# Kernel optimization log

Hardware: AMD Instinct MI355X
Metric: run time of the kernel (lower is better)

## Reference

```python
import jax, jax.numpy as jnp
import numpy as np

TAU = 0.5

def setup_inputs() -> dict:
    key = jax.random.key(0)
    kx, ky = jax.random.split(key)
    B, H = 8192, 256
    x = jax.random.normal(kx, (B, H), dtype=jnp.float32)
    y = jax.random.normal(ky, (B, H), dtype=jnp.float32)
    return {"x": x, "y": y}

def reference(x, y):
    # L2-normalize rows
    x_norm = x / jnp.linalg.norm(x, axis=1, keepdims=True)
    y_norm = y / jnp.linalg.norm(y, axis=1, keepdims=True)
    xy_norm = jnp.concatenate([x_norm, y_norm], axis=0)  # [2N, H]
    yx_norm = jnp.concatenate([y_norm, x_norm], axis=0)  # [2N, H]
    # [2N, 2N] cosine-similarity matrix (dominant memory traffic)
    sim_mat_1 = xy_norm @ xy_norm.T
    exp_mat = jnp.exp(sim_mat_1 / TAU)
    exp_row_sum = jnp.sum(exp_mat, axis=1)
    exp_diag = jnp.diagonal(exp_mat)
    denominator = exp_row_sum - exp_diag
    # diag(xy_norm @ yx_norm.T) is the row-wise dot product (avoids redundant NxN matmul)
    pos_sim = jnp.sum(xy_norm * yx_norm, axis=1)
    numerator = jnp.exp(pos_sim / TAU)
    nt_xent = -jnp.log(numerator / denominator)
    return jnp.mean(nt_xent)
```

## Files before the change

kernel.cpp:

```cpp
#include <hip/hip_runtime.h>
#include <hip/hip_bf16.h>
#include <math.h>

constexpr int NROWS = 8192;
constexpr int HDIM  = 256;
constexpr int N2    = 16384;
constexpr int BM    = 128;
constexpr int NTILE = N2 / BM;
constexpr int NBLK  = NTILE * (NTILE + 1) / 2;

constexpr float PRESCALE = 1.69864357f;

typedef __attribute__((ext_vector_type(4))) float floatx4;
typedef __attribute__((ext_vector_type(8))) short shortx8;

#define DPP_ADD(v, CTRL) do {                                                \
    union { float f; int i; } _u, _r; _u.f = (v);                            \
    _r.i = __builtin_amdgcn_update_dpp(0, _u.i, (CTRL), 0xF, 0xF, true);     \
    (v) += _r.f; } while (0)
#define DPP_ROW_SUM16(v) do { DPP_ADD(v,0x101); DPP_ADD(v,0x102);            \
    DPP_ADD(v,0x104); DPP_ADD(v,0x108); } while (0)
#define DPP_ALL_SUM16(v) do { DPP_ADD(v,0xB1); DPP_ADD(v,0x4E);              \
    DPP_ADD(v,0x124); DPP_ADD(v,0x128); } while (0)


__global__ __launch_bounds__(256) void normalize_kernel(
    const float* __restrict__ x, const float* __restrict__ y,
    __hip_bfloat16* __restrict__ Zp, float* __restrict__ pos,
    float* __restrict__ rowsum, float* __restrict__ out)
{
    const int wave = threadIdx.x >> 6, lane = threadIdx.x & 63;
    const int row  = blockIdx.x * 4 + wave;

    const float4 xv = ((const float4*)x)[row * 64 + lane];
    const float4 yv = ((const float4*)y)[row * 64 + lane];

    float sx  = xv.x*xv.x + xv.y*xv.y + xv.z*xv.z + xv.w*xv.w;
    float sy  = yv.x*yv.x + yv.y*yv.y + yv.z*yv.z + yv.w*yv.w;
    float sxy = xv.x*yv.x + xv.y*yv.y + xv.z*yv.z + xv.w*yv.w;
    DPP_ALL_SUM16(sx); DPP_ALL_SUM16(sy); DPP_ALL_SUM16(sxy);
    sx  += __shfl_xor(sx, 16);  sx  += __shfl_xor(sx, 32);
    sy  += __shfl_xor(sy, 16);  sy  += __shfl_xor(sy, 32);
    sxy += __shfl_xor(sxy, 16); sxy += __shfl_xor(sxy, 32);

    const float rxn = rsqrtf(sx), ryn = rsqrtf(sy);
    const float rx = rxn * PRESCALE, ry = ryn * PRESCALE;

    union { ushort4 u; __hip_bfloat16 h[4]; } zx, zy;
    zx.h[0] = __float2bfloat16(xv.x * rx); zx.h[1] = __float2bfloat16(xv.y * rx);
    zx.h[2] = __float2bfloat16(xv.z * rx); zx.h[3] = __float2bfloat16(xv.w * rx);
    zy.h[0] = __float2bfloat16(yv.x * ry); zy.h[1] = __float2bfloat16(yv.y * ry);
    zy.h[2] = __float2bfloat16(yv.z * ry); zy.h[3] = __float2bfloat16(yv.w * ry);

    const int tile = row >> 4, m = row & 15;
    const size_t off = (size_t)tile * 4096 + (lane >> 1) * 128 + m * 8 + (lane & 1) * 4;
    *(ushort4*)(Zp + off)                 = zx.u;
    *(ushort4*)(Zp + off + 512 * 4096)    = zy.u;

    if (lane == 0) {
        const float p = sxy * rxn * ryn;
        pos[row]         = p;
        pos[row + NROWS] = p;
    }
    const int gt = blockIdx.x * 256 + threadIdx.x;
    if (gt < N2) rowsum[gt] = 0.f;
    if (gt == 0) out[0] = 0.f;
}

__global__ __launch_bounds__(256, 3) void simgemm_kernel(
    const __hip_bfloat16* __restrict__ Zp, float* __restrict__ rowsum)
{
    const int b = blockIdx.x;
    const int k = b & 7;
    const int m = b >> 3;
    int bi, bj;
    if (m < 136) {
        int ti = (int)((33.0f - sqrtf(1089.0f - 8.0f * (float)m)) * 0.5f);
        if (m < ti * (33 - ti) / 2) ti--;
        else if (m >= (ti + 1) * (32 - ti) / 2) ti++;
        const int tj = ti + (m - ti * (33 - ti) / 2);
        bi = k * 16 + ti;
        bj = k * 16 + tj;
    } else {
        const int m2 = m - 136;
        const int hh = m2 >> 7;
        const int r  = m2 & 127;
        const int h  = hh * 8 + k;
        const int q  = h >> 1;
        const int sub = h & 1;
        int gi = 0;
        #pragma unroll
        for (int t = 6; t > 0; --t)
            if (q >= t * (15 - t) / 2) { gi = t; break; }
        const int gj = gi + 1 + (q - gi * (15 - gi) / 2);
        bi = gi * 16 + sub * 8 + (r >> 4);
        bj = gj * 16 + (r & 15);
    }
    const bool diag = (bi == bj);

    __shared__ float rs[BM];
    __shared__ float cs[BM];

    const int tid  = threadIdx.x;
    const int wave = tid >> 6;
    const int lane = tid & 63;
    const int wm   = wave & 1;
    const int wn   = wave >> 1;
    const int g    = lane >> 4;
    const int m15  = lane & 15;

    if (tid < BM) { rs[tid] = 0.f; cs[tid] = 0.f; }
    __syncthreads();

    const __hip_bfloat16* pA = Zp + (size_t)(bi * 8 + wm * 4) * 4096 + lane * 8;
    const __hip_bfloat16* pB = Zp + (size_t)(bj * 8 + wn * 4) * 4096 + lane * 8;

    floatx4 acc[4][4] = {};
    shortx8 af[3][4], bf[3][4];

    #pragma unroll
    for (int f = 0; f < 4; ++f) {
        af[0][f] = *(const shortx8*)(pA + f * 4096);
        bf[0][f] = *(const shortx8*)(pB + f * 4096);
    }
    #pragma unroll
    for (int f = 0; f < 4; ++f) {
        af[1][f] = *(const shortx8*)(pA + f * 4096 + 512);
        bf[1][f] = *(const shortx8*)(pB + f * 4096 + 512);
    }

    #pragma unroll
    for (int s = 0; s < HDIM / 32; ++s) {
        const int cur = s % 3;
        if (s + 2 < HDIM / 32) {
            const int nxt = (s + 2) % 3;
            #pragma unroll
            for (int f = 0; f < 4; ++f) {
                af[nxt][f] = *(const shortx8*)(pA + f * 4096 + (s + 2) * 512);
                bf[nxt][f] = *(const shortx8*)(pB + f * 4096 + (s + 2) * 512);
            }
        }
        #pragma unroll
        for (int fm = 0; fm < 4; ++fm)
            #pragma unroll
            for (int fn = 0; fn < 4; ++fn)
                acc[fm][fn] = __builtin_amdgcn_mfma_f32_16x16x32_bf16(
                    af[cur][fm], bf[cur][fn], acc[fm][fn], 0, 0, 0);
    }

    float rp[4][4] = {{0.f}};
    float cp[4]    = {0.f};

    if (!diag) {
        #pragma unroll
        for (int fm = 0; fm < 4; ++fm)
            #pragma unroll
            for (int fn = 0; fn < 4; ++fn) {
                const floatx4 a = acc[fm][fn];
                #pragma unroll
                for (int q = 0; q < 4; ++q) {
                    const float e = __builtin_amdgcn_exp2f(a[q]);
                    rp[fm][q] += e;
                    cp[fn]    += e;
                }
            }
    } else {
        #pragma unroll
        for (int fm = 0; fm < 4; ++fm)
            #pragma unroll
            for (int fn = 0; fn < 4; ++fn) {
                const floatx4 a = acc[fm][fn];
                const int cl = wn * 64 + fn * 16 + m15;
                #pragma unroll
                for (int q = 0; q < 4; ++q) {
                    const int rl = wm * 64 + fm * 16 + g * 4 + q;
                    float e = __builtin_amdgcn_exp2f(a[q]);
                    if (cl <= rl) e = 0.f;
                    rp[fm][q] += e;
                    cp[fn]    += e;
                }
            }
    }

    #pragma unroll
    for (int fm = 0; fm < 4; ++fm)
        #pragma unroll
        for (int q = 0; q < 4; ++q) {
            float v = rp[fm][q];
            DPP_ROW_SUM16(v);
            rp[fm][q] = v;
        }
    if (m15 == 0) {
        #pragma unroll
        for (int fm = 0; fm < 4; ++fm)
            #pragma unroll
            for (int q = 0; q < 4; ++q)
                atomicAdd(&rs[wm * 64 + fm * 16 + g * 4 + q], rp[fm][q]);
    }

    #pragma unroll
    for (int mask = 16; mask < 64; mask <<= 1)
        #pragma unroll
        for (int fn = 0; fn < 4; ++fn)
            cp[fn] += __shfl_xor(cp[fn], mask);
    if (g == 0) {
        #pragma unroll
        for (int fn = 0; fn < 4; ++fn)
            atomicAdd(&cs[wn * 64 + fn * 16 + m15], cp[fn]);
    }

    __syncthreads();
    if (tid < BM) {
        atomicAdd(&rowsum[(size_t)bi * BM + tid], rs[tid]);
        atomicAdd(&rowsum[(size_t)bj * BM + tid], cs[tid]);
    }
}

__global__ __launch_bounds__(1024) void finalize_kernel(
    const float* __restrict__ rowsum, const float* __restrict__ pos,
    float* __restrict__ out)
{
    const int i = threadIdx.x + blockIdx.x * 1024;
    float s = logf(rowsum[i]) - 2.0f * pos[i];
    #pragma unroll
    for (int off = 32; off; off >>= 1) s += __shfl_down(s, off);
    __shared__ float sh[16];
    const int lt = threadIdx.x;
    if ((lt & 63) == 0) sh[lt >> 6] = s;
    __syncthreads();
    if (lt == 0) {
        float tot = 0.f;
        #pragma unroll
        for (int w = 0; w < 16; ++w) tot += sh[w];
        atomicAdd(out, tot / (float)N2);
    }
}

extern "C" void kernel_launch(void* const* d_in, const int* in_sizes, int n_in,
                              void* d_out, int out_size, void* d_ws, size_t ws_size,
                              hipStream_t stream)
{
    const float* x = (const float*)d_in[0];
    const float* y = (const float*)d_in[1];

    __hip_bfloat16* Zp = (__hip_bfloat16*)d_ws;
    float* rowsum = (float*)((char*)d_ws + (size_t)N2 * HDIM * sizeof(__hip_bfloat16));
    float* pos    = rowsum + N2;

    normalize_kernel<<<NROWS / 4, 256, 0, stream>>>(x, y, Zp, pos, rowsum, (float*)d_out);
    simgemm_kernel<<<NBLK, 256, 0, stream>>>(Zp, rowsum);
    finalize_kernel<<<N2 / 1024, 1024, 0, stream>>>(rowsum, pos, (float*)d_out);
}
```

Measured before the change: 165.7 us.

## Switch similarity GEMM operands from bf16 to fp8 e4m3 MFMA

The normalize kernel now writes the normalized rows, scaled by 16, as fp8 e4m3 bytes instead of bf16, keeping the same interleaved tile layout. The GEMM loads 8-byte operand fragments and uses the fp8 16x16x32 MFMA. Each accumulator is rescaled before exp2 to undo the operand scaling and apply the temperature. This halves operand bytes fetched from cache and memory and uses the higher-rate fp8 matrix path, and the launch-bounds occupancy hint is raised from 3 to 4. The trade is lower dot-product precision, which may push the loss outside tolerance, plus one extra multiply per element in the exp epilogue.

Result: no change. 163.3 us (-1.4%).

```diff
diff --git a/kernel.cpp b/kernel.cpp
--- a/kernel.cpp
+++ b/kernel.cpp
@@ -1,5 +1,6 @@
 #include <hip/hip_runtime.h>
 #include <hip/hip_bf16.h>
+#include <hip/hip_fp8.h>
 #include <math.h>
 
 constexpr int NROWS = 8192;
@@ -9,10 +10,10 @@
 constexpr int NTILE = N2 / BM;
 constexpr int NBLK  = NTILE * (NTILE + 1) / 2;
 
-constexpr float PRESCALE = 1.69864357f;
+constexpr float ZSCALE    = 16.0f;
+constexpr float ACC2EXP2  = 2.885390082f / 256.0f;
 
 typedef __attribute__((ext_vector_type(4))) float floatx4;
-typedef __attribute__((ext_vector_type(8))) short shortx8;
 
 #define DPP_ADD(v, CTRL) do {                                                \
     union { float f; int i; } _u, _r; _u.f = (v);                            \
@@ -26,7 +27,7 @@
 
 __global__ __launch_bounds__(256) void normalize_kernel(
     const float* __restrict__ x, const float* __restrict__ y,
-    __hip_bfloat16* __restrict__ Zp, float* __restrict__ pos,
+    unsigned char* __restrict__ Zp8, float* __restrict__ pos,
     float* __restrict__ rowsum, float* __restrict__ out)
 {
     const int wave = threadIdx.x >> 6, lane = threadIdx.x & 63;
@@ -44,18 +45,20 @@
     sxy += __shfl_xor(sxy, 16); sxy += __shfl_xor(sxy, 32);
 
     const float rxn = rsqrtf(sx), ryn = rsqrtf(sy);
-    const float rx = rxn * PRESCALE, ry = ryn * PRESCALE;
-
-    union { ushort4 u; __hip_bfloat16 h[4]; } zx, zy;
-    zx.h[0] = __float2bfloat16(xv.x * rx); zx.h[1] = __float2bfloat16(xv.y * rx);
-    zx.h[2] = __float2bfloat16(xv.z * rx); zx.h[3] = __float2bfloat16(xv.w * rx);
-    zy.h[0] = __float2bfloat16(yv.x * ry); zy.h[1] = __float2bfloat16(yv.y * ry);
-    zy.h[2] = __float2bfloat16(yv.z * ry); zy.h[3] = __float2bfloat16(yv.w * ry);
+    const float rx = rxn * ZSCALE, ry = ryn * ZSCALE;
+
+    auto pack4 = [](float a, float b, float c, float d) -> unsigned int {
+        __hip_fp8_e4m3 f0(a), f1(b), f2(c), f3(d);
+        return (unsigned int)f0.__x | ((unsigned int)f1.__x << 8) |
+               ((unsigned int)f2.__x << 16) | ((unsigned int)f3.__x << 24);
+    };
+    const unsigned int wx = pack4(xv.x * rx, xv.y * rx, xv.z * rx, xv.w * rx);
+    const unsigned int wy = pack4(yv.x * ry, yv.y * ry, yv.z * ry, yv.w * ry);
 
     const int tile = row >> 4, m = row & 15;
     const size_t off = (size_t)tile * 4096 + (lane >> 1) * 128 + m * 8 + (lane & 1) * 4;
-    *(ushort4*)(Zp + off)                 = zx.u;
-    *(ushort4*)(Zp + off + 512 * 4096)    = zy.u;
+    *(unsigned int*)(Zp8 + off)                         = wx;
+    *(unsigned int*)(Zp8 + off + (size_t)512 * 4096)    = wy;
 
     if (lane == 0) {
         const float p = sxy * rxn * ryn;
@@ -67,8 +70,8 @@
     if (gt == 0) out[0] = 0.f;
 }
 
-__global__ __launch_bounds__(256, 3) void simgemm_kernel(
-    const __hip_bfloat16* __restrict__ Zp, float* __restrict__ rowsum)
+__global__ __launch_bounds__(256, 4) void simgemm_kernel(
+    const unsigned char* __restrict__ Zp8, float* __restrict__ rowsum)
 {
     const int b = blockIdx.x;
     const int k = b & 7;
@@ -112,21 +115,21 @@
     if (tid < BM) { rs[tid] = 0.f; cs[tid] = 0.f; }
     __syncthreads();
 
-    const __hip_bfloat16* pA = Zp + (size_t)(bi * 8 + wm * 4) * 4096 + lane * 8;
-    const __hip_bfloat16* pB = Zp + (size_t)(bj * 8 + wn * 4) * 4096 + lane * 8;
+    const unsigned char* pA = Zp8 + (size_t)(bi * 8 + wm * 4) * 4096 + lane * 8;
+    const unsigned char* pB = Zp8 + (size_t)(bj * 8 + wn * 4) * 4096 + lane * 8;
 
     floatx4 acc[4][4] = {};
-    shortx8 af[3][4], bf[3][4];
+    long af[3][4], bf[3][4];
 
     #pragma unroll
     for (int f = 0; f < 4; ++f) {
-        af[0][f] = *(const shortx8*)(pA + f * 4096);
-        bf[0][f] = *(const shortx8*)(pB + f * 4096);
+        af[0][f] = *(const long*)(pA + f * 4096);
+        bf[0][f] = *(const long*)(pB + f * 4096);
     }
     #pragma unroll
     for (int f = 0; f < 4; ++f) {
-        af[1][f] = *(const shortx8*)(pA + f * 4096 + 512);
-        bf[1][f] = *(const shortx8*)(pB + f * 4096 + 512);
+        af[1][f] = *(const long*)(pA + f * 4096 + 512);
+        bf[1][f] = *(const long*)(pB + f * 4096 + 512);
     }
 
     #pragma unroll
@@ -136,15 +139,15 @@
             const int nxt = (s + 2) % 3;
             #pragma unroll
             for (int f = 0; f < 4; ++f) {
-                af[nxt][f] = *(const shortx8*)(pA + f * 4096 + (s + 2) * 512);
-                bf[nxt][f] = *(const shortx8*)(pB + f * 4096 + (s + 2) * 512);
+                af[nxt][f] = *(const long*)(pA + f * 4096 + (s + 2) * 512);
+                bf[nxt][f] = *(const long*)(pB + f * 4096 + (s + 2) * 512);
             }
         }
         #pragma unroll
         for (int fm = 0; fm < 4; ++fm)
             #pragma unroll
             for (int fn = 0; fn < 4; ++fn)
-                acc[fm][fn] = __builtin_amdgcn_mfma_f32_16x16x32_bf16(
+                acc[fm][fn] = __builtin_amdgcn_mfma_f32_16x16x32_fp8_fp8(
                     af[cur][fm], bf[cur][fn], acc[fm][fn], 0, 0, 0);
     }
 
@@ -159,7 +162,7 @@
                 const floatx4 a = acc[fm][fn];
                 #pragma unroll
                 for (int q = 0; q < 4; ++q) {
-                    const float e = __builtin_amdgcn_exp2f(a[q]);
+                    const float e = __builtin_amdgcn_exp2f(a[q] * ACC2EXP2);
                     rp[fm][q] += e;
                     cp[fn]    += e;
                 }
@@ -174,7 +177,7 @@
                 #pragma unroll
                 for (int q = 0; q < 4; ++q) {
                     const int rl = wm * 64 + fm * 16 + g * 4 + q;
-                    float e = __builtin_amdgcn_exp2f(a[q]);
+                    float e = __builtin_amdgcn_exp2f(a[q] * ACC2EXP2);
                     if (cl <= rl) e = 0.f;
                     rp[fm][q] += e;
                     cp[fn]    += e;
@@ -243,11 +246,11 @@
     const float* x = (const float*)d_in[0];
     const float* y = (const float*)d_in[1];
 
-    __hip_bfloat16* Zp = (__hip_bfloat16*)d_ws;
-    float* rowsum = (float*)((char*)d_ws + (size_t)N2 * HDIM * sizeof(__hip_bfloat16));
+    unsigned char* Zp8 = (unsigned char*)d_ws;
+    float* rowsum = (float*)((char*)d_ws + (size_t)N2 * HDIM);
     float* pos    = rowsum + N2;
 
-    normalize_kernel<<<NROWS / 4, 256, 0, stream>>>(x, y, Zp, pos, rowsum, (float*)d_out);
-    simgemm_kernel<<<NBLK, 256, 0, stream>>>(Zp, rowsum);
+    normalize_kernel<<<NROWS / 4, 256, 0, stream>>>(x, y, Zp8, pos, rowsum, (float*)d_out);
+    simgemm_kernel<<<NBLK, 256, 0, stream>>>(Zp8, rowsum);
     finalize_kernel<<<N2 / 1024, 1024, 0, stream>>>(rowsum, pos, (float*)d_out);
 }
```
